# Performance work log

Hardware: AMD Instinct MI355X
Metric: run time of the kernel (lower is better)

## Reference

```python
import jax, jax.numpy as jnp
import numpy as np

THRESHOLD = 0.0

def setup_inputs() -> dict:
    key = jax.random.key(0)
    k1, k2 = jax.random.split(key)
    B, N, D = 16384, 16384, 128
    query_embeddings = jax.random.normal(k1, (B, D), dtype=jnp.float32)
    # module normalizes learned centroids; emulate for provided centroids too-faithfulness
    # NOTE: forward itself does NOT normalize provided cluster_embeddings, so we pass raw randn
    cluster_embeddings = jax.random.normal(k2, (N, D), dtype=jnp.float32)
    return {"query_embeddings": query_embeddings,
            "cluster_embeddings": cluster_embeddings,
            "top_k": 8}

def reference(query_embeddings, cluster_embeddings, top_k):
    # cosine similarity path: plain matmul (B, N)
    all_similarities = jnp.matmul(query_embeddings, cluster_embeddings.T)
    k = min(int(top_k), all_similarities.shape[1])
    top_k_similarities, top_k_indices = jax.lax.top_k(all_similarities, k)
    mask = top_k_similarities >= THRESHOLD
    cluster_ids = jnp.where(mask, top_k_indices, -1)
    return (cluster_ids, top_k_similarities, all_similarities)
```

## Files before the change

### kernel.cpp

```cpp
#include <hip/hip_runtime.h>
#include <math.h>

#define NROWS 16384
#define NCOLS 16384
#define DIM   128
#define TM    128
#define TN    64
#define NSPLIT 4
#define CPS   (NCOLS/NSPLIT)
#define NCH   (CPS/TN)
#define KP    8

typedef __attribute__((ext_vector_type(8))) short bf16x8;
typedef __attribute__((ext_vector_type(4))) float f32x4;

__device__ __forceinline__ unsigned short bf16_rne(float x) {
  unsigned u = __float_as_uint(x);
  unsigned r = u + 0x7fffu + ((u >> 16) & 1u);
  return (unsigned short)(r >> 16);
}

#define BAR() do {                                   \
  __builtin_amdgcn_sched_barrier(0);                 \
  asm volatile("s_waitcnt lgkmcnt(0)" ::: "memory"); \
  __builtin_amdgcn_s_barrier();                      \
  __builtin_amdgcn_sched_barrier(0);                 \
} while (0)

__global__ __launch_bounds__(256) void split_kernel(
    const float* __restrict__ C, unsigned char* __restrict__ Cimg)
{
  const unsigned u = blockIdx.x * 256 + threadIdx.x;
  const int c  = u & 16383;
  const int kk = u >> 14;
  const f32x4* src = (const f32x4*)(C + (size_t)c * DIM + kk * 16);
  f32x4 f[4];
  f[0] = src[0]; f[1] = src[1]; f[2] = src[2]; f[3] = src[3];
  const unsigned chunkbase = ((unsigned)(c >> 6)) << 15;
  const unsigned T = ((((unsigned)c >> 4) & 3u) << 2) | ((unsigned)kk >> 1);
  #pragma unroll
  for (int s = 0; s < 2; ++s) {
    bf16x8 h, l;
    #pragma unroll
    for (int e = 0; e < 8; ++e) {
      float x = f[s * 2 + (e >> 2)][e & 3];
      unsigned short hb = bf16_rne(x);
      float xh = __uint_as_float((unsigned)hb << 16);
      l[e] = (short)bf16_rne(x - xh);
      h[e] = (short)hb;
    }
    unsigned ln  = (unsigned)(c & 15) | ((((unsigned)kk * 2 + s) & 3u) << 4);
    unsigned off = chunkbase + (T << 10) + (ln << 4);
    *(bf16x8*)&Cimg[off]          = h;
    *(bf16x8*)&Cimg[off + 16384u] = l;
  }
}

__global__ __launch_bounds__(512, 4) void sim_topk_kernel(
    const float* __restrict__ Q, const unsigned char* __restrict__ Cimg,
    float* __restrict__ S, int* __restrict__ cand)
{
  __shared__ __align__(16) unsigned char lds[65536];
  const int t = threadIdx.x;
  const int w = t >> 6, lane = t & 63;

  const int bid = blockIdx.x;
  const int xcd = bid & 7;
  const int cs  = xcd >> 1;
  const int rb  = ((xcd & 1) << 6) | (bid >> 3);
  const int row0 = rb * TM;
  const int col0 = cs * CPS;
  const int phase = rb & (NCH - 1);

  const int arow = row0 + w * 16 + (lane & 15);
  bf16x8 ah[4], al[4];
  {
    const f32x4* Q4 = (const f32x4*)(Q + (size_t)arow * DIM);
    #pragma unroll
    for (int ks = 0; ks < 4; ++ks) {
      f32x4 x0 = Q4[ks * 8 + (lane >> 4) * 2];
      f32x4 x1 = Q4[ks * 8 + (lane >> 4) * 2 + 1];
      #pragma unroll
      for (int e = 0; e < 8; ++e) {
        float x = (e < 4) ? x0[e & 3] : x1[e & 3];
        unsigned short hb = bf16_rne(x);
        float xh = __uint_as_float((unsigned)hb << 16);
        al[ks][e] = (short)bf16_rne(x - xh);
        ah[ks][e] = (short)hb;
      }
    }
  }

  f32x4 st[4];
  auto gload = [&](int ch) {
    const f32x4* p = (const f32x4*)(Cimg + (((size_t)(cs * NCH + ch)) << 15)) + t;
    st[0] = p[0]; st[1] = p[512]; st[2] = p[1024]; st[3] = p[1536];
  };
  auto swrite = [&](unsigned buf) {
    #pragma unroll
    for (int r = 0; r < 4; ++r)
      *(f32x4*)&lds[buf + (unsigned)r * 8192u + (unsigned)t * 16u] = st[r];
  };

  gload(phase); swrite(0u); gload((phase + 1) & (NCH - 1));
  BAR();

  float tv[KP]; int ti[KP];
  #pragma unroll
  for (int j = 0; j < KP; ++j) { tv[j] = -INFINITY; ti[j] = 0x7fffffff; }

  for (int i = 0; i < NCH; ++i) {
    const int ch = (phase + i) & (NCH - 1);
    const unsigned cur = (i & 1) ? 32768u : 0u;
    const int colg0 = col0 + ch * TN;

    if (i + 1 < NCH) swrite(cur ^ 32768u);
    if (i + 2 < NCH) gload((phase + i + 2) & (NCH - 1));

    f32x4 acc[4];
    #pragma unroll
    for (int c = 0; c < 4; ++c) acc[c] = {0.f, 0.f, 0.f, 0.f};
    #pragma unroll
    for (int ks = 0; ks < 4; ++ks) {
      #pragma unroll
      for (int cbk = 0; cbk < 4; ++cbk) {
        unsigned o = cur + ((unsigned)(cbk * 4 + ks) << 10) + ((unsigned)lane << 4);
        bf16x8 bh = *(const bf16x8*)&lds[o];
        bf16x8 bl = *(const bf16x8*)&lds[o + 16384u];
        acc[cbk] = __builtin_amdgcn_mfma_f32_16x16x32_bf16(bh, ah[ks], acc[cbk], 0, 0, 0);
        acc[cbk] = __builtin_amdgcn_mfma_f32_16x16x32_bf16(bl, ah[ks], acc[cbk], 0, 0, 0);
        acc[cbk] = __builtin_amdgcn_mfma_f32_16x16x32_bf16(bh, al[ks], acc[cbk], 0, 0, 0);
      }
    }

    {
      const int cloc = (lane >> 4) * 4;
      float* sp = &S[(size_t)arow * NCOLS + colg0 + cloc];
      #pragma unroll
      for (int cbk = 0; cbk < 4; ++cbk) {
        *(f32x4*)&sp[cbk * 16] = acc[cbk];
        #pragma unroll
        for (int e = 0; e < 4; ++e) {
          float val = acc[cbk][e];
          if (val > tv[KP - 1]) {
            tv[KP - 1] = val; ti[KP - 1] = colg0 + cbk * 16 + cloc + e;
            #pragma unroll
            for (int m = KP - 1; m > 0; --m) {
              if (tv[m] > tv[m - 1]) {
                float q = tv[m]; tv[m] = tv[m - 1]; tv[m - 1] = q;
                int   x = ti[m]; ti[m] = ti[m - 1]; ti[m - 1] = x;
              }
            }
          }
        }
      }
    }
    BAR();
  }

  #pragma unroll
  for (int off = 16; off <= 32; off <<= 1) {
    float ov[KP]; int ox[KP];
    #pragma unroll
    for (int j = 0; j < KP; ++j) {
      ov[j] = __shfl_xor(tv[j], off);
      ox[j] = __shfl_xor(ti[j], off);
    }
    #pragma unroll
    for (int j = 0; j < KP; ++j) {
      if (ov[j] > tv[KP - 1] || (ov[j] == tv[KP - 1] && ox[j] < ti[KP - 1])) {
        tv[KP - 1] = ov[j]; ti[KP - 1] = ox[j];
        #pragma unroll
        for (int m = KP - 1; m > 0; --m) {
          if (tv[m] > tv[m - 1] || (tv[m] == tv[m - 1] && ti[m] < ti[m - 1])) {
            float q = tv[m]; tv[m] = tv[m - 1]; tv[m - 1] = q;
            int   x = ti[m]; ti[m] = ti[m - 1]; ti[m - 1] = x;
          }
        }
      }
    }
  }
  if (lane < 16) {
    int* dst = cand + ((size_t)arow * NSPLIT + cs) * KP;
    #pragma unroll
    for (int j = 0; j < KP; ++j) dst[j] = ti[j];
  }
}

__global__ __launch_bounds__(256) void rerank_kernel(
    const float* __restrict__ Q, const float* __restrict__ C,
    const int* __restrict__ cand, float* __restrict__ out)
{
  const int t = threadIdx.x, w = t >> 6, lane = t & 63;
  const int r = blockIdx.x * 4 + w;
  const f32x4* Q4 = (const f32x4*)(Q + (size_t)r * DIM);

  int cidx = 0;
  if (lane < 32) cidx = cand[(size_t)r * 32 + lane];
  const f32x4* C4 = (const f32x4*)(C + (size_t)cidx * DIM);

  double acc = 0.0;
  #pragma unroll 8
  for (int d4 = 0; d4 < 32; ++d4) {
    f32x4 q = Q4[d4];
    f32x4 c = C4[d4];
    acc += (double)q[0] * (double)c[0];
    acc += (double)q[1] * (double)c[1];
    acc += (double)q[2] * (double)c[2];
    acc += (double)q[3] * (double)c[3];
  }

  double mv = (lane < 32) ? acc : -1.0e300;
  int    mi = (lane < 32) ? cidx : 0x7fffffff;

  float* oi = out;
  float* os = out + (size_t)NROWS * 8;

  for (int k = 0; k < 8; ++k) {
    double bv = mv; int bi = mi;
    #pragma unroll
    for (int off = 32; off >= 1; off >>= 1) {
      double ov = __shfl_xor(bv, off);
      int    o2 = __shfl_xor(bi, off);
      if (ov > bv || (ov == bv && o2 < bi)) { bv = ov; bi = o2; }
    }
    if (lane == 0) {
      os[(size_t)r * 8 + k] = (float)bv;
      oi[(size_t)r * 8 + k] = (bv >= 0.0) ? (float)bi : -1.0f;
    }
    if (mi == bi) mv = -1.0e300;
  }
}

extern "C" void kernel_launch(void* const* d_in, const int* in_sizes, int n_in,
                              void* d_out, int out_size, void* d_ws, size_t ws_size,
                              hipStream_t stream) {
  const float* Q = (const float*)d_in[0];
  const float* C = (const float*)d_in[1];
  float* out = (float*)d_out;
  float* S   = out + (size_t)2 * NROWS * 8;

  unsigned char* Cimg = (unsigned char*)d_ws;
  int* cand = (int*)(Cimg + 8388608);

  split_kernel<<<dim3(512), dim3(256), 0, stream>>>(C, Cimg);
  sim_topk_kernel<<<dim3((NROWS / TM) * NSPLIT), dim3(512), 0, stream>>>(Q, Cimg, S, cand);
  rerank_kernel<<<dim3(NROWS / 4), dim3(256), 0, stream>>>(Q, C, cand, out);
}
```

Baseline: 557.1 us.

## Use single bf16 MFMA pass with packed-key top-16 and wider fp64 rerank

```diff
diff --git a/kernel.cpp b/kernel.cpp
--- a/kernel.cpp
+++ b/kernel.cpp
@@ -9,7 +9,7 @@
 #define NSPLIT 4
 #define CPS   (NCOLS/NSPLIT)
 #define NCH   (CPS/TN)
-#define KP    8
+#define KP    16
 
 typedef __attribute__((ext_vector_type(8))) short bf16x8;
 typedef __attribute__((ext_vector_type(4))) float f32x4;
@@ -20,11 +20,22 @@
   return (unsigned short)(r >> 16);
 }
 
-#define BAR() do {                                   \
-  __builtin_amdgcn_sched_barrier(0);                 \
-  asm volatile("s_waitcnt lgkmcnt(0)" ::: "memory"); \
-  __builtin_amdgcn_s_barrier();                      \
-  __builtin_amdgcn_sched_barrier(0);                 \
+__device__ __forceinline__ unsigned mkkey(float v, int col) {
+  unsigned b = __float_as_uint(v);
+  unsigned u = b ^ (unsigned)(((int)b >> 31) | (int)0x80000000);
+  return (u & 0xFFFFC000u) | (unsigned)(16383 - col);
+}
+
+#define INSERT(tk, key) do {                                                  \
+  unsigned _k = (key);                                                        \
+  if (_k > tk[KP - 1]) {                                                      \
+    tk[KP - 1] = _k;                                                          \
+    _Pragma("unroll")                                                         \
+    for (int _m = KP - 1; _m > 0; --_m)                                       \
+      if (tk[_m] > tk[_m - 1]) {                                              \
+        unsigned _q = tk[_m]; tk[_m] = tk[_m - 1]; tk[_m - 1] = _q;           \
+      }                                                                       \
+  }                                                                           \
 } while (0)
 
 __global__ __launch_bounds__(256) void split_kernel(
@@ -36,23 +47,16 @@
   const f32x4* src = (const f32x4*)(C + (size_t)c * DIM + kk * 16);
   f32x4 f[4];
   f[0] = src[0]; f[1] = src[1]; f[2] = src[2]; f[3] = src[3];
-  const unsigned chunkbase = ((unsigned)(c >> 6)) << 15;
+  const unsigned chunkbase = ((unsigned)(c >> 6)) << 14;
   const unsigned T = ((((unsigned)c >> 4) & 3u) << 2) | ((unsigned)kk >> 1);
   #pragma unroll
   for (int s = 0; s < 2; ++s) {
-    bf16x8 h, l;
-    #pragma unroll
-    for (int e = 0; e < 8; ++e) {
-      float x = f[s * 2 + (e >> 2)][e & 3];
-      unsigned short hb = bf16_rne(x);
-      float xh = __uint_as_float((unsigned)hb << 16);
-      l[e] = (short)bf16_rne(x - xh);
-      h[e] = (short)hb;
-    }
-    unsigned ln  = (unsigned)(c & 15) | ((((unsigned)kk * 2 + s) & 3u) << 4);
-    unsigned off = chunkbase + (T << 10) + (ln << 4);
-    *(bf16x8*)&Cimg[off]          = h;
-    *(bf16x8*)&Cimg[off + 16384u] = l;
+    bf16x8 h;
+    #pragma unroll
+    for (int e = 0; e < 8; ++e)
+      h[e] = (short)bf16_rne(f[s * 2 + (e >> 2)][e & 3]);
+    unsigned ln = (unsigned)(c & 15) | ((((unsigned)kk * 2 + s) & 3u) << 4);
+    *(bf16x8*)&Cimg[chunkbase + (T << 10) + (ln << 4)] = h;
   }
 }
 
@@ -60,9 +64,10 @@
     const float* __restrict__ Q, const unsigned char* __restrict__ Cimg,
     float* __restrict__ S, int* __restrict__ cand)
 {
-  __shared__ __align__(16) unsigned char lds[65536];
+  __shared__ unsigned mlds[TM * 2 * KP];
   const int t = threadIdx.x;
   const int w = t >> 6, lane = t & 63;
+  const int wr = w >> 1, wc = w & 1;
 
   const int bid = blockIdx.x;
   const int xcd = bid & 7;
@@ -72,118 +77,84 @@
   const int col0 = cs * CPS;
   const int phase = rb & (NCH - 1);
 
-  const int arow = row0 + w * 16 + (lane & 15);
-  bf16x8 ah[4], al[4];
+  const int arow0 = row0 + wr * 32 + (lane & 15);
+  const int arow1 = arow0 + 16;
+  bf16x8 a0h[4], a1h[4];
   {
-    const f32x4* Q4 = (const f32x4*)(Q + (size_t)arow * DIM);
+    const f32x4* Qp0 = (const f32x4*)(Q + (size_t)arow0 * DIM) + (lane >> 4) * 2;
+    const f32x4* Qp1 = (const f32x4*)(Q + (size_t)arow1 * DIM) + (lane >> 4) * 2;
     #pragma unroll
     for (int ks = 0; ks < 4; ++ks) {
-      f32x4 x0 = Q4[ks * 8 + (lane >> 4) * 2];
-      f32x4 x1 = Q4[ks * 8 + (lane >> 4) * 2 + 1];
+      f32x4 x0 = Qp0[ks * 8], x1 = Qp0[ks * 8 + 1];
+      f32x4 y0 = Qp1[ks * 8], y1 = Qp1[ks * 8 + 1];
       #pragma unroll
       for (int e = 0; e < 8; ++e) {
-        float x = (e < 4) ? x0[e & 3] : x1[e & 3];
-        unsigned short hb = bf16_rne(x);
-        float xh = __uint_as_float((unsigned)hb << 16);
-        al[ks][e] = (short)bf16_rne(x - xh);
-        ah[ks][e] = (short)hb;
+        a0h[ks][e] = (short)bf16_rne((e < 4) ? x0[e & 3] : x1[e & 3]);
+        a1h[ks][e] = (short)bf16_rne((e < 4) ? y0[e & 3] : y1[e & 3]);
       }
     }
   }
 
-  f32x4 st[4];
-  auto gload = [&](int ch) {
-    const f32x4* p = (const f32x4*)(Cimg + (((size_t)(cs * NCH + ch)) << 15)) + t;
-    st[0] = p[0]; st[1] = p[512]; st[2] = p[1024]; st[3] = p[1536];
-  };
-  auto swrite = [&](unsigned buf) {
-    #pragma unroll
-    for (int r = 0; r < 4; ++r)
-      *(f32x4*)&lds[buf + (unsigned)r * 8192u + (unsigned)t * 16u] = st[r];
-  };
-
-  gload(phase); swrite(0u); gload((phase + 1) & (NCH - 1));
-  BAR();
-
-  float tv[KP]; int ti[KP];
+  unsigned tk0[KP], tk1[KP];
   #pragma unroll
-  for (int j = 0; j < KP; ++j) { tv[j] = -INFINITY; ti[j] = 0x7fffffff; }
+  for (int j = 0; j < KP; ++j) { tk0[j] = 0u; tk1[j] = 0u; }
 
   for (int i = 0; i < NCH; ++i) {
     const int ch = (phase + i) & (NCH - 1);
-    const unsigned cur = (i & 1) ? 32768u : 0u;
-    const int colg0 = col0 + ch * TN;
-
-    if (i + 1 < NCH) swrite(cur ^ 32768u);
-    if (i + 2 < NCH) gload((phase + i + 2) & (NCH - 1));
-
-    f32x4 acc[4];
-    #pragma unroll
-    for (int c = 0; c < 4; ++c) acc[c] = {0.f, 0.f, 0.f, 0.f};
-    #pragma unroll
-    for (int ks = 0; ks < 4; ++ks) {
+    const bf16x8* bp = (const bf16x8*)(Cimg + (((size_t)(cs * NCH + ch)) << 14));
+    const int colg0 = col0 + ch * TN + wc * 32;
+
+    #pragma unroll
+    for (int cb = 0; cb < 2; ++cb) {
+      f32x4 acc0 = {0.f, 0.f, 0.f, 0.f};
+      f32x4 acc1 = {0.f, 0.f, 0.f, 0.f};
       #pragma unroll
-      for (int cbk = 0; cbk < 4; ++cbk) {
-        unsigned o = cur + ((unsigned)(cbk * 4 + ks) << 10) + ((unsigned)lane << 4);
-        bf16x8 bh = *(const bf16x8*)&lds[o];
-        bf16x8 bl = *(const bf16x8*)&lds[o + 16384u];
-        acc[cbk] = __builtin_amdgcn_mfma_f32_16x16x32_bf16(bh, ah[ks], acc[cbk], 0, 0, 0);
-        acc[cbk] = __builtin_amdgcn_mfma_f32_16x16x32_bf16(bl, ah[ks], acc[cbk], 0, 0, 0);
-        acc[cbk] = __builtin_amdgcn_mfma_f32_16x16x32_bf16(bh, al[ks], acc[cbk], 0, 0, 0);
+      for (int ks = 0; ks < 4; ++ks) {
+        bf16x8 bh = bp[(((wc * 2 + cb) * 4 + ks) << 6) + lane];
+        acc0 = __builtin_amdgcn_mfma_f32_16x16x32_bf16(bh, a0h[ks], acc0, 0, 0, 0);
+        acc1 = __builtin_amdgcn_mfma_f32_16x16x32_bf16(bh, a1h[ks], acc1, 0, 0, 0);
       }
-    }
-
-    {
-      const int cloc = (lane >> 4) * 4;
-      float* sp = &S[(size_t)arow * NCOLS + colg0 + cloc];
+      const int cbase = colg0 + cb * 16 + (lane >> 4) * 4;
+      *(f32x4*)&S[(size_t)arow0 * NCOLS + cbase] = acc0;
+      *(f32x4*)&S[(size_t)arow1 * NCOLS + cbase] = acc1;
       #pragma unroll
-      for (int cbk = 0; cbk < 4; ++cbk) {
-        *(f32x4*)&sp[cbk * 16] = acc[cbk];
-        #pragma unroll
-        for (int e = 0; e < 4; ++e) {
-          float val = acc[cbk][e];
-          if (val > tv[KP - 1]) {
-            tv[KP - 1] = val; ti[KP - 1] = colg0 + cbk * 16 + cloc + e;
-            #pragma unroll
-            for (int m = KP - 1; m > 0; --m) {
-              if (tv[m] > tv[m - 1]) {
-                float q = tv[m]; tv[m] = tv[m - 1]; tv[m - 1] = q;
-                int   x = ti[m]; ti[m] = ti[m - 1]; ti[m - 1] = x;
-              }
-            }
-          }
-        }
+      for (int e = 0; e < 4; ++e) {
+        INSERT(tk0, mkkey(acc0[e], cbase + e));
+        INSERT(tk1, mkkey(acc1[e], cbase + e));
       }
     }
-    BAR();
   }
 
   #pragma unroll
   for (int off = 16; off <= 32; off <<= 1) {
-    float ov[KP]; int ox[KP];
+    unsigned o0[KP], o1[KP];
     #pragma unroll
     for (int j = 0; j < KP; ++j) {
-      ov[j] = __shfl_xor(tv[j], off);
-      ox[j] = __shfl_xor(ti[j], off);
-    }
+      o0[j] = (unsigned)__shfl_xor((int)tk0[j], off);
+      o1[j] = (unsigned)__shfl_xor((int)tk1[j], off);
+    }
+    #pragma unroll
+    for (int j = 0; j < KP; ++j) { INSERT(tk0, o0[j]); INSERT(tk1, o1[j]); }
+  }
+
+  if (lane < 16) {
+    const int r0 = wr * 32 + lane, r1 = r0 + 16;
     #pragma unroll
     for (int j = 0; j < KP; ++j) {
-      if (ov[j] > tv[KP - 1] || (ov[j] == tv[KP - 1] && ox[j] < ti[KP - 1])) {
-        tv[KP - 1] = ov[j]; ti[KP - 1] = ox[j];
-        #pragma unroll
-        for (int m = KP - 1; m > 0; --m) {
-          if (tv[m] > tv[m - 1] || (tv[m] == tv[m - 1] && ti[m] < ti[m - 1])) {
-            float q = tv[m]; tv[m] = tv[m - 1]; tv[m - 1] = q;
-            int   x = ti[m]; ti[m] = ti[m - 1]; ti[m - 1] = x;
-          }
-        }
-      }
-    }
-  }
-  if (lane < 16) {
-    int* dst = cand + ((size_t)arow * NSPLIT + cs) * KP;
-    #pragma unroll
-    for (int j = 0; j < KP; ++j) dst[j] = ti[j];
+      mlds[(r0 * 2 + wc) * KP + j] = tk0[j];
+      mlds[(r1 * 2 + wc) * KP + j] = tk1[j];
+    }
+  }
+  __syncthreads();
+  if (t < TM) {
+    unsigned best[KP];
+    #pragma unroll
+    for (int j = 0; j < KP; ++j) best[j] = mlds[(t * 2) * KP + j];
+    #pragma unroll
+    for (int j = 0; j < KP; ++j) INSERT(best, mlds[(t * 2 + 1) * KP + j]);
+    int* dst = cand + ((size_t)(row0 + t) * NSPLIT + cs) * KP;
+    #pragma unroll
+    for (int j = 0; j < KP; ++j) dst[j] = 16383 - (int)(best[j] & 0x3FFFu);
   }
 }
 
@@ -195,8 +166,7 @@
   const int r = blockIdx.x * 4 + w;
   const f32x4* Q4 = (const f32x4*)(Q + (size_t)r * DIM);
 
-  int cidx = 0;
-  if (lane < 32) cidx = cand[(size_t)r * 32 + lane];
+  const int cidx = cand[(size_t)r * (NSPLIT * KP) + lane];
   const f32x4* C4 = (const f32x4*)(C + (size_t)cidx * DIM);
 
   double acc = 0.0;
@@ -210,8 +180,8 @@
     acc += (double)q[3] * (double)c[3];
   }
 
-  double mv = (lane < 32) ? acc : -1.0e300;
-  int    mi = (lane < 32) ? cidx : 0x7fffffff;
+  double mv = acc;
+  int    mi = cidx;
 
   float* oi = out;
   float* os = out + (size_t)NROWS * 8;
@@ -241,7 +211,7 @@
   float* S   = out + (size_t)2 * NROWS * 8;
 
   unsigned char* Cimg = (unsigned char*)d_ws;
-  int* cand = (int*)(Cimg + 8388608);
+  int* cand = (int*)(Cimg + 4194304);
 
   split_kernel<<<dim3(512), dim3(256), 0, stream>>>(C, Cimg);
   sim_topk_kernel<<<dim3((NROWS / TM) * NSPLIT), dim3(512), 0, stream>>>(Q, Cimg, S, cand);
```

Result: slower. 683.2 us (+22.6%).
